# Kernel tuning notes

Measured on AMD Instinct MI355X. Metric: run time of the kernel, lower is better.

Reference implementation:

```python
import jax, jax.numpy as jnp
import numpy as np

BS, C_IN, NP, NA = 2, 64, 1024, 60
NA_OUT, KS, ANN = 60, 3, 8
C_OUT = 128


def setup_inputs() -> dict:
    key = jax.random.key(0)
    k1, k2, k3, k4 = jax.random.split(key, 4)
    feats = jax.random.normal(k1, (BS, C_IN, NP, NA), dtype=jnp.float32)
    # precomputed anchor-neighbor weights, normalized over the ann axis
    w = jax.random.uniform(k2, (NA_OUT, KS, ANN), dtype=jnp.float32)
    intra_w = w / jnp.sum(w, axis=-1, keepdims=True)
    intra_idx = jax.random.randint(k3, (NA_OUT, KS, ANN), 0, NA)
    # xavier-normal-ish weight for the basic conv, flattened [C_OUT, C_IN*KS]
    W = jax.random.normal(k4, (C_OUT, C_IN * KS), dtype=jnp.float32) * (2.0 / np.sqrt(C_IN * KS + C_OUT))
    bias = jnp.full((1, C_OUT, 1), 0.001, dtype=jnp.float32)
    return {"feats": feats, "intra_w": intra_w, "W": W, "bias": bias, "intra_idx": intra_idx}


def reference(feats, intra_w, W, bias, intra_idx):
    bs, c, npts, na = feats.shape
    na_out, ks, ann = intra_idx.shape
    dim_out = W.shape[0]
    # intra_zpconv_grouping_naive: gather over anchor axis then weighted sum over ann
    g = feats[:, :, :, intra_idx]                      # [b, c, p, o, k, a]
    grouped = jnp.einsum('bcpoka,oka->bckpo', g, intra_w)  # [b, c, ks, p, na_out]
    # BasicZPConv: view to [b, c*ks, p*na_out], W @ x + bias
    x = grouped.reshape(bs, c * ks, npts * na_out)
    out = jnp.einsum('oi,bin->bon', W, x) + bias       # [b, dim_out, p*na_out]
    return out.reshape(bs, dim_out, npts, na_out)
```

## Files before the change

kernel.cpp:

```cpp
#include <hip/hip_runtime.h>

#define NPTS 1024
#define NA   60
#define CIN  64
#define KSZ  3
#define ANN  8
#define COUT 128
#define KD   192

using bf16x8 = __attribute__((ext_vector_type(8))) short;
using f32x4  = __attribute__((ext_vector_type(4))) float;

__device__ __forceinline__ unsigned short f2bf(float f) {
    unsigned int u = __builtin_bit_cast(unsigned int, f);
    u += 0x7FFFu + ((u >> 16) & 1u);
    return (unsigned short)(u >> 16);
}

__global__ void build_tables(const float* __restrict__ intra_w,
                             const float* __restrict__ W,
                             const int*   __restrict__ intra_idx,
                             unsigned short* __restrict__ ws) {
    int f = blockIdx.x * 256 + threadIdx.x;
    if (f < 24576) {
        int j = f & 7, l = (f >> 3) & 63, x = f >> 9;
        int kt = x % 6, mt = x / 6;
        int m  = mt * 16 + (l & 15);
        int ip = kt * 32 + 8 * (l >> 4) + j;
        int c  = ip & 63, ks = ip >> 6;
        ws[f] = f2bf(W[m * KD + c * KSZ + ks]);
    } else if (f < 36864) {
        int f2 = f - 24576;
        int j = f2 & 7, l = (f2 >> 3) & 63;
        int kt = (f2 >> 9) & 1, nt = f2 >> 10;
        int np = nt * 16 + (l & 15);
        int ap = kt * 32 + 8 * (l >> 4) + j;
        float s = 0.f;
        if (np < 180 && ap < 60) {
            int ks = (np >= 120) ? 2 : ((np >= 60) ? 1 : 0);
            int o  = np - 60 * ks;
            const int*   ix = intra_idx + (o * KSZ + ks) * ANN;
            const float* wx = intra_w   + (o * KSZ + ks) * ANN;
            #pragma unroll
            for (int a = 0; a < ANN; a++) s += (ix[a] == ap) ? wx[a] : 0.f;
        }
        ws[f] = f2bf(s);
    }
}

__global__ __launch_bounds__(256, 3)
void intrazp_mfma(const float* __restrict__ feats,
                  const float* __restrict__ bias,
                  const unsigned short* __restrict__ ws,
                  float* __restrict__ out) {
    __shared__ __align__(16) unsigned short AsT[64 * 192];

    const int t    = threadIdx.x;
    const int wave = t >> 6, lane = t & 63;
    const int l15  = lane & 15, g = lane >> 4;
    const int bp   = blockIdx.x;
    const int b    = bp >> 10, p = bp & 1023;

    #pragma unroll
    for (int r = 0; r < 3; r++) AsT[60 * 192 + r * 256 + t] = 0;

    const unsigned short* Sfrag = ws + 24576;
    const int wm = wave & 1, wn = wave >> 1;

    bf16x8 a1[2][2];
    {
        const float* fb = feats + ((size_t)b * CIN * NPTS + p) * NA;
        #pragma unroll
        for (int mi = 0; mi < 2; mi++) {
            int c = (2 * wm + mi) * 16 + l15;
            const float* fr = fb + (size_t)c * NPTS * NA;
            #pragma unroll
            for (int kt = 0; kt < 2; kt++) {
                int a0 = kt * 32 + 8 * g;
                float4 lo = *(const float4*)(fr + a0);
                int ah = a0 + 4;
                float4 hi = *(const float4*)(fr + ((ah < NA) ? ah : 0));
                bf16x8 v;
                v[0] = (short)f2bf(lo.x); v[1] = (short)f2bf(lo.y);
                v[2] = (short)f2bf(lo.z); v[3] = (short)f2bf(lo.w);
                v[4] = (short)f2bf(hi.x); v[5] = (short)f2bf(hi.y);
                v[6] = (short)f2bf(hi.z); v[7] = (short)f2bf(hi.w);
                a1[mi][kt] = v;
            }
        }
    }

    #pragma unroll
    for (int ni = 0; ni < 6; ni++) {
        int nt = wn * 6 + ni;
        bf16x8 b0 = *(const bf16x8*)(Sfrag + ((nt * 2 + 0) * 64 + lane) * 8);
        bf16x8 b1 = *(const bf16x8*)(Sfrag + ((nt * 2 + 1) * 64 + lane) * 8);

        int np = nt * 16 + l15;
        int ks = (np >= 120) ? 2 : ((np >= 60) ? 1 : 0);
        int o  = np - 60 * ks;
        int sw = (o & 7) << 4;
        int rowbyte = o * 384;

        #pragma unroll
        for (int mi = 0; mi < 2; mi++) {
            f32x4 acc = {0.f, 0.f, 0.f, 0.f};
            acc = __builtin_amdgcn_mfma_f32_16x16x32_bf16(a1[mi][0], b0, acc, 0, 0, 0);
            acc = __builtin_amdgcn_mfma_f32_16x16x32_bf16(a1[mi][1], b1, acc, 0, 0, 0);
            if (np < 180) {
                int cbase = (2 * wm + mi) * 16 + 4 * g;
                int ipb   = ks * 64 + cbase;
                unsigned int lo = (unsigned int)f2bf(acc[0]) | ((unsigned int)f2bf(acc[1]) << 16);
                unsigned int hi = (unsigned int)f2bf(acc[2]) | ((unsigned int)f2bf(acc[3]) << 16);
                int byte = (rowbyte + ipb * 2) ^ sw;
                *(uint2*)((char*)AsT + byte) = make_uint2(lo, hi);
            }
        }
    }

    __syncthreads();

    const int wm2 = wave & 1, wn2 = wave >> 1;

    bf16x8 b2a[6], b2b[6];
    {
        int o0 = (2 * wn2 + 0) * 16 + l15;
        int o1 = (2 * wn2 + 1) * 16 + l15;
        int rb0 = o0 * 384, sw0 = (o0 & 7) << 4;
        int rb1 = o1 * 384, sw1 = (o1 & 7) << 4;
        #pragma unroll
        for (int kt = 0; kt < 6; kt++) {
            int x = (kt * 32 + 8 * g) * 2;
            b2a[kt] = *(const bf16x8*)((char*)AsT + ((rb0 + x) ^ sw0));
            b2b[kt] = *(const bf16x8*)((char*)AsT + ((rb1 + x) ^ sw1));
        }
    }

    const int o0 = (2 * wn2 + 0) * 16 + l15;
    const int o1 = (2 * wn2 + 1) * 16 + l15;

    #pragma unroll
    for (int mj = 0; mj < 4; mj++) {
        int mt = wm2 * 4 + mj;
        f32x4 accA = {0.f, 0.f, 0.f, 0.f};
        f32x4 accB = {0.f, 0.f, 0.f, 0.f};
        #pragma unroll
        for (int kt = 0; kt < 6; kt++) {
            bf16x8 a2 = *(const bf16x8*)(ws + ((mt * 6 + kt) * 64 + lane) * 8);
            accA = __builtin_amdgcn_mfma_f32_16x16x32_bf16(a2, b2a[kt], accA, 0, 0, 0);
            accB = __builtin_amdgcn_mfma_f32_16x16x32_bf16(a2, b2b[kt], accB, 0, 0, 0);
        }
        int cbase = mt * 16 + 4 * g;
        float bv0 = bias[cbase + 0], bv1 = bias[cbase + 1];
        float bv2 = bias[cbase + 2], bv3 = bias[cbase + 3];
        float* ob = out + (((size_t)b * COUT + cbase) * NPTS + p) * NA;
        const size_t cs = (size_t)NPTS * NA;
        if (o0 < NA) {
            ob[0 * cs + o0] = accA[0] + bv0;
            ob[1 * cs + o0] = accA[1] + bv1;
            ob[2 * cs + o0] = accA[2] + bv2;
            ob[3 * cs + o0] = accA[3] + bv3;
        }
        if (o1 < NA) {
            ob[0 * cs + o1] = accB[0] + bv0;
            ob[1 * cs + o1] = accB[1] + bv1;
            ob[2 * cs + o1] = accB[2] + bv2;
            ob[3 * cs + o1] = accB[3] + bv3;
        }
    }
}

extern "C" void kernel_launch(void* const* d_in, const int* in_sizes, int n_in,
                              void* d_out, int out_size, void* d_ws, size_t ws_size,
                              hipStream_t stream) {
    const float* feats     = (const float*)d_in[0];
    const float* intra_w   = (const float*)d_in[1];
    const float* W         = (const float*)d_in[2];
    const float* bias      = (const float*)d_in[3];
    const int*   intra_idx = (const int*)d_in[4];
    float* out = (float*)d_out;
    unsigned short* ws = (unsigned short*)d_ws;

    build_tables<<<dim3(144), dim3(256), 0, stream>>>(intra_w, W, intra_idx, ws);
    intrazp_mfma<<<dim3(2 * NPTS), dim3(256), 0, stream>>>(feats, bias, ws, out);
}
```

Before: 120.3 us.

## Remap second GEMM so each wave owns full N, hoist weight fragment loads

The second MFMA stage is repartitioned so each wave computes 2 M-tiles across all 4 N-tiles, loading its W fragments from global once before the barrier instead of reloading them inside the loop. The stage-one selection fragments are also loaded up front into registers. The occupancy hint is raised from 3 to 4 blocks per CU. Hoisting more fragments into registers increases register pressure, which may conflict with the higher occupancy target and cause spills.

Result: no change. 122.1 us (+1.4%).

```diff
diff --git a/kernel.cpp b/kernel.cpp
--- a/kernel.cpp
+++ b/kernel.cpp
@@ -48,7 +48,7 @@
     }
 }
 
-__global__ __launch_bounds__(256, 3)
+__global__ __launch_bounds__(256, 4)
 void intrazp_mfma(const float* __restrict__ feats,
                   const float* __restrict__ bias,
                   const unsigned short* __restrict__ ws,
@@ -66,6 +66,11 @@
 
     const unsigned short* Sfrag = ws + 24576;
     const int wm = wave & 1, wn = wave >> 1;
+
+    bf16x8 bfr[12];
+    #pragma unroll
+    for (int i = 0; i < 12; i++)
+        bfr[i] = *(const bf16x8*)(Sfrag + ((wn * 12 + i) * 64 + lane) * 8);
 
     bf16x8 a1[2][2];
     {
@@ -93,9 +98,6 @@
     #pragma unroll
     for (int ni = 0; ni < 6; ni++) {
         int nt = wn * 6 + ni;
-        bf16x8 b0 = *(const bf16x8*)(Sfrag + ((nt * 2 + 0) * 64 + lane) * 8);
-        bf16x8 b1 = *(const bf16x8*)(Sfrag + ((nt * 2 + 1) * 64 + lane) * 8);
-
         int np = nt * 16 + l15;
         int ks = (np >= 120) ? 2 : ((np >= 60) ? 1 : 0);
         int o  = np - 60 * ks;
@@ -105,8 +107,8 @@
         #pragma unroll
         for (int mi = 0; mi < 2; mi++) {
             f32x4 acc = {0.f, 0.f, 0.f, 0.f};
-            acc = __builtin_amdgcn_mfma_f32_16x16x32_bf16(a1[mi][0], b0, acc, 0, 0, 0);
-            acc = __builtin_amdgcn_mfma_f32_16x16x32_bf16(a1[mi][1], b1, acc, 0, 0, 0);
+            acc = __builtin_amdgcn_mfma_f32_16x16x32_bf16(a1[mi][0], bfr[ni * 2 + 0], acc, 0, 0, 0);
+            acc = __builtin_amdgcn_mfma_f32_16x16x32_bf16(a1[mi][1], bfr[ni * 2 + 1], acc, 0, 0, 0);
             if (np < 180) {
                 int cbase = (2 * wm + mi) * 16 + 4 * g;
                 int ipb   = ks * 64 + cbase;
@@ -118,54 +120,59 @@
         }
     }
 
+    bf16x8 a2[2][6];
+    #pragma unroll
+    for (int mi = 0; mi < 2; mi++)
+        #pragma unroll
+        for (int kt = 0; kt < 6; kt++)
+            a2[mi][kt] = *(const bf16x8*)(ws + (((wave * 2 + mi) * 6 + kt) * 64 + lane) * 8);
+
     __syncthreads();
 
-    const int wm2 = wave & 1, wn2 = wave >> 1;
-
-    bf16x8 b2a[6], b2b[6];
-    {
-        int o0 = (2 * wn2 + 0) * 16 + l15;
-        int o1 = (2 * wn2 + 1) * 16 + l15;
-        int rb0 = o0 * 384, sw0 = (o0 & 7) << 4;
-        int rb1 = o1 * 384, sw1 = (o1 & 7) << 4;
-        #pragma unroll
-        for (int kt = 0; kt < 6; kt++) {
-            int x = (kt * 32 + 8 * g) * 2;
-            b2a[kt] = *(const bf16x8*)((char*)AsT + ((rb0 + x) ^ sw0));
-            b2b[kt] = *(const bf16x8*)((char*)AsT + ((rb1 + x) ^ sw1));
-        }
+    int rb[4], swz[4], ov[4];
+    #pragma unroll
+    for (int nt = 0; nt < 4; nt++) {
+        int o = nt * 16 + l15;
+        ov[nt]  = o;
+        rb[nt]  = o * 384;
+        swz[nt] = (o & 7) << 4;
     }
 
-    const int o0 = (2 * wn2 + 0) * 16 + l15;
-    const int o1 = (2 * wn2 + 1) * 16 + l15;
+    f32x4 acc[2][4];
+    #pragma unroll
+    for (int mi = 0; mi < 2; mi++)
+        #pragma unroll
+        for (int nt = 0; nt < 4; nt++) acc[mi][nt] = (f32x4){0.f, 0.f, 0.f, 0.f};
 
     #pragma unroll
-    for (int mj = 0; mj < 4; mj++) {
-        int mt = wm2 * 4 + mj;
-        f32x4 accA = {0.f, 0.f, 0.f, 0.f};
-        f32x4 accB = {0.f, 0.f, 0.f, 0.f};
+    for (int kt = 0; kt < 6; kt++) {
+        int x = (kt * 32 + 8 * g) * 2;
+        bf16x8 bb[4];
         #pragma unroll
-        for (int kt = 0; kt < 6; kt++) {
-            bf16x8 a2 = *(const bf16x8*)(ws + ((mt * 6 + kt) * 64 + lane) * 8);
-            accA = __builtin_amdgcn_mfma_f32_16x16x32_bf16(a2, b2a[kt], accA, 0, 0, 0);
-            accB = __builtin_amdgcn_mfma_f32_16x16x32_bf16(a2, b2b[kt], accB, 0, 0, 0);
-        }
-        int cbase = mt * 16 + 4 * g;
+        for (int nt = 0; nt < 4; nt++)
+            bb[nt] = *(const bf16x8*)((char*)AsT + ((rb[nt] + x) ^ swz[nt]));
+        #pragma unroll
+        for (int mi = 0; mi < 2; mi++)
+            #pragma unroll
+            for (int nt = 0; nt < 4; nt++)
+                acc[mi][nt] = __builtin_amdgcn_mfma_f32_16x16x32_bf16(a2[mi][kt], bb[nt], acc[mi][nt], 0, 0, 0);
+    }
+
+    #pragma unroll
+    for (int mi = 0; mi < 2; mi++) {
+        int cbase = (wave * 2 + mi) * 16 + 4 * g;
         float bv0 = bias[cbase + 0], bv1 = bias[cbase + 1];
         float bv2 = bias[cbase + 2], bv3 = bias[cbase + 3];
         float* ob = out + (((size_t)b * COUT + cbase) * NPTS + p) * NA;
         const size_t cs = (size_t)NPTS * NA;
-        if (o0 < NA) {
-            ob[0 * cs + o0] = accA[0] + bv0;
-            ob[1 * cs + o0] = accA[1] + bv1;
-            ob[2 * cs + o0] = accA[2] + bv2;
-            ob[3 * cs + o0] = accA[3] + bv3;
-        }
-        if (o1 < NA) {
-            ob[0 * cs + o1] = accB[0] + bv0;
-            ob[1 * cs + o1] = accB[1] + bv1;
-            ob[2 * cs + o1] = accB[2] + bv2;
-            ob[3 * cs + o1] = accB[3] + bv3;
+        #pragma unroll
+        for (int nt = 0; nt < 4; nt++) {
+            if (ov[nt] < NA) {
+                ob[0 * cs + ov[nt]] = acc[mi][nt][0] + bv0;
+                ob[1 * cs + ov[nt]] = acc[mi][nt][1] + bv1;
+                ob[2 * cs + ov[nt]] = acc[mi][nt][2] + bv2;
+                ob[3 * cs + ov[nt]] = acc[mi][nt][3] + bv3;
+            }
         }
     }
 }
```
